# Performance work log

Hardware: AMD Instinct MI355X
Metric: run time of the kernel (lower is better)

## Reference

```python
import jax, jax.numpy as jnp
import numpy as np

_ELECTRODE_POSITIONS = jnp.array([[0.3, 0.25, 0.0], [-0.3, 0.25, 0.0], [-0.05, -0.4, 0.0],
                                  [0.03, 0.05, 0.2], [0.0, 0.05, 0.22], [-0.04, 0.01, 0.21],
                                  [-0.08, -0.02, 0.18], [-0.14, -0.02, 0.13], [-0.2, -0.02, 0.07]],
                                 dtype=jnp.float32)

B, N, T, K, H = 8, 1024, 512, 9, 32


def setup_inputs() -> dict:
    key = jax.random.key(0)
    ks = jax.random.split(key, 9)
    d = jax.random.normal(ks[1], (B, N, 3), jnp.float32)
    d = d / jnp.linalg.norm(d, axis=-1, keepdims=True)  # unit dipole directions
    return {
        'position': jax.random.normal(ks[0], (B, N, 3), jnp.float32) * 0.1,
        'dipole_dir': d,
        'amplitude': jax.random.uniform(ks[2], (B, N), jnp.float32),
        'envelope_t': jax.random.normal(ks[3], (B, N, T), jnp.float32),
        'electrode_offset': jax.random.normal(ks[4], (B, K, 3), jnp.float32) * 0.01,
        'W1': jax.random.normal(ks[5], (H, 7), jnp.float32) * 0.3,
        'b1': jax.random.normal(ks[6], (H,), jnp.float32) * 0.1,
        'W2': jax.random.normal(ks[7], (1, H), jnp.float32) * 0.3,
        'b2': jax.random.normal(ks[8], (1,), jnp.float32) * 0.1,
    }


def _attenuation(position, E, W1, b1, W2, b2):
    # position [B,N,3], E [B,K,3] -> correction [B,N,K]
    pos_exp = jnp.broadcast_to(position[:, :, None, :], (B, N, K, 3))
    r_vec = E[:, None, :, :] - position[:, :, None, :]          # [B,N,K,3]
    r_dist = jnp.maximum(jnp.linalg.norm(r_vec, axis=-1, keepdims=True), 1e-6)
    r_hat = r_vec / r_dist
    feat = jnp.concatenate([pos_exp, r_hat, r_dist], axis=-1)   # [B,N,K,7]
    h = jax.nn.gelu(jnp.einsum('bnkf,hf->bnkh', feat, W1) + b1, approximate=False)
    raw = (jnp.einsum('bnkh,oh->bnko', h, W2) + b2)[..., 0]     # [B,N,K]
    return 1.0 + jnp.tanh(raw) * 0.5


def reference(position, dipole_dir, amplitude, envelope_t, electrode_offset, W1, b1, W2, b2):
    E = _ELECTRODE_POSITIONS[None] + electrode_offset            # [B,K,3]
    amp_env = (amplitude[..., None] * envelope_t)[:, :, None, :]  # [B,N,1,T]
    moment = dipole_dir[..., None] * amp_env                     # [B,N,3,T]
    r_vec = E[:, None, :, :] - position[:, :, None, :]           # [B,N,K,3]
    EPS_SQ = 0.04
    r_dist_sq = jnp.sum(r_vec ** 2, axis=-1)                     # [B,N,K]
    atten_denom = (r_dist_sq + EPS_SQ) ** 1.5
    correction = _attenuation(position, E, W1, b1, W2, b2)       # [B,N,K]
    dot = jnp.einsum('bndt,bnkd->bnkt', moment, r_vec)           # [B,N,K,T]
    V_per_gaussian = dot * (correction / atten_denom)[..., None]
    V_electrodes = jnp.clip(jnp.sum(V_per_gaussian, axis=1), -50.0, 50.0)  # [B,K,T]
    V_RA, V_LA, V_LL = V_electrodes[:, 0], V_electrodes[:, 1], V_electrodes[:, 2]
    V_chest = V_electrodes[:, 3:9]
    WCT = (V_RA + V_LA + V_LL) / 3.0
    leads = jnp.stack([V_LA - V_RA, V_LL - V_RA, V_LL - V_LA,
                       -(V_LA + V_LL) / 2.0 + V_RA,
                       V_LA - (V_RA + V_LL) / 2.0,
                       V_LL - (V_RA + V_LA) / 2.0], axis=1)
    chest_leads = V_chest - WCT[:, None, :]
    v_leads = jnp.concatenate([leads, chest_leads], axis=1)      # [B,12,T]
    return v_leads, V_electrodes
```

## Files before the change

### kernel.cpp

```cpp
#include <hip/hip_runtime.h>
#include <hip/hip_bf16.h>
#include <math.h>

#define BB 8
#define NN 1024
#define TT 512
#define KK 9
#define HH 32

#define NCHUNK 64
#define NPER   (NN/NCHUNK)

__constant__ float c_epos[KK][3] = {
    { 0.30f,  0.25f, 0.00f},
    {-0.30f,  0.25f, 0.00f},
    {-0.05f, -0.40f, 0.00f},
    { 0.03f,  0.05f, 0.20f},
    { 0.00f,  0.05f, 0.22f},
    {-0.04f,  0.01f, 0.21f},
    {-0.08f, -0.02f, 0.18f},
    {-0.14f, -0.02f, 0.13f},
    {-0.20f, -0.02f, 0.07f},
};

__global__ __launch_bounds__(256) void fused_kernel(
    const float* __restrict__ pos,
    const float* __restrict__ dd,
    const float* __restrict__ amp,
    const float* __restrict__ env,
    const float* __restrict__ eoff,
    const float* __restrict__ W1,
    const float* __restrict__ pb1,
    const float* __restrict__ W2,
    const float* __restrict__ pb2,
    float* __restrict__ partial)
{
    const int tid   = threadIdx.x;
    const int chunk = blockIdx.x;
    const int b     = blockIdx.y;
    const int n0    = chunk * NPER;

    __shared__ float sW1[HH * 7];
    __shared__ float sb1[HH];
    __shared__ float sW2[HH];
    __shared__ float sb2;
    __shared__ float sE[KK][3];
    __shared__ float sA[NPER][12];

    if (tid < HH * 7) sW1[tid] = W1[tid];
    if (tid < HH)     { sb1[tid] = pb1[tid]; sW2[tid] = W2[tid]; }
    if (tid < KK * 3) sE[tid / 3][tid % 3] = c_epos[tid / 3][tid % 3] + eoff[b * KK * 3 + tid];
    if (tid == 0)     sb2 = pb2[0];
    __syncthreads();

    if (tid < NPER * KK) {
        const int k  = tid % KK;
        const int nl = tid / KK;
        const int bn = b * NN + n0 + nl;

        const float px = pos[bn * 3 + 0];
        const float py = pos[bn * 3 + 1];
        const float pz = pos[bn * 3 + 2];

        const float rx = sE[k][0] - px, ry = sE[k][1] - py, rz = sE[k][2] - pz;
        const float r2 = rx * rx + ry * ry + rz * rz;
        const float d0 = r2 + 0.04f;
        const float denom = d0 * sqrtf(d0);

        const float rdist = fmaxf(sqrtf(r2), 1e-6f);
        const float rinv  = 1.0f / rdist;
        float feat[7];
        feat[0] = px; feat[1] = py; feat[2] = pz;
        feat[3] = rx * rinv; feat[4] = ry * rinv; feat[5] = rz * rinv;
        feat[6] = rdist;

        float raw = sb2;
        #pragma unroll
        for (int j = 0; j < HH; ++j) {
            float s = sb1[j];
            #pragma unroll
            for (int f = 0; f < 7; ++f) s += sW1[j * 7 + f] * feat[f];
            const float g = 0.5f * s * (1.0f + erff(s * 0.70710678118654752f));
            raw += sW2[j] * g;
        }
        const float corr = 1.0f + 0.5f * tanhf(raw);

        const float ddx = dd[bn * 3 + 0], ddy = dd[bn * 3 + 1], ddz = dd[bn * 3 + 2];
        const float dot = ddx * rx + ddy * ry + ddz * rz;

        sA[nl][k] = amp[bn] * dot * corr / denom;
    }
    __syncthreads();

    float2 acc[KK];
    #pragma unroll
    for (int k = 0; k < KK; ++k) { acc[k].x = 0.0f; acc[k].y = 0.0f; }

    const float2* envp = (const float2*)(env + ((size_t)(b * NN + n0)) * TT) + tid;
    const float4* s4 = (const float4*)sA;
    #pragma unroll
    for (int nl = 0; nl < NPER; ++nl) {
        const float2 ev = envp[(size_t)nl * (TT / 2)];
        const float4 a0 = s4[nl * 3 + 0];
        const float4 a1 = s4[nl * 3 + 1];
        const float  a8 = sA[nl][8];
        acc[0].x += a0.x * ev.x; acc[0].y += a0.x * ev.y;
        acc[1].x += a0.y * ev.x; acc[1].y += a0.y * ev.y;
        acc[2].x += a0.z * ev.x; acc[2].y += a0.z * ev.y;
        acc[3].x += a0.w * ev.x; acc[3].y += a0.w * ev.y;
        acc[4].x += a1.x * ev.x; acc[4].y += a1.x * ev.y;
        acc[5].x += a1.y * ev.x; acc[5].y += a1.y * ev.y;
        acc[6].x += a1.z * ev.x; acc[6].y += a1.z * ev.y;
        acc[7].x += a1.w * ev.x; acc[7].y += a1.w * ev.y;
        acc[8].x += a8   * ev.x; acc[8].y += a8   * ev.y;
    }

    float2* pp = (float2*)(partial + (((size_t)chunk * BB + b) * KK) * TT) + tid;
    #pragma unroll
    for (int k = 0; k < KK; ++k) pp[(size_t)k * (TT / 2)] = acc[k];
}

__global__ __launch_bounds__(256) void finalize_kernel(
    const float* __restrict__ partial,
    float* __restrict__ out)
{
    const int tid = threadIdx.x;
    const int tl4 = tid & 7;
    const int cg  = tid >> 3;
    const int tc  = blockIdx.x;
    const int b   = blockIdx.y;
    const int t0  = tc * 32;

    float4 s[KK];
    #pragma unroll
    for (int k = 0; k < KK; ++k) s[k] = make_float4(0.f, 0.f, 0.f, 0.f);

    #pragma unroll
    for (int ci = 0; ci < 2; ++ci) {
        const int c = cg + 32 * ci;
        const float* base = partial + (((size_t)c * BB + b) * KK) * TT + t0 + tl4 * 4;
        #pragma unroll
        for (int k = 0; k < KK; ++k) {
            const float4 v = *(const float4*)(base + (size_t)k * TT);
            s[k].x += v.x; s[k].y += v.y; s[k].z += v.z; s[k].w += v.w;
        }
    }

    __shared__ float4 sV[32][KK][8];
    __shared__ float  sRf[KK][32];
    #pragma unroll
    for (int k = 0; k < KK; ++k) sV[cg][k][tl4] = s[k];
    __syncthreads();

    if (tid < KK * 8) {
        const int k  = tid >> 3;
        const int tl = tid & 7;
        float4 v = make_float4(0.f, 0.f, 0.f, 0.f);
        #pragma unroll
        for (int g = 0; g < 32; ++g) {
            const float4 u = sV[g][k][tl];
            v.x += u.x; v.y += u.y; v.z += u.z; v.w += u.w;
        }
        sRf[k][tl * 4 + 0] = fminf(fmaxf(v.x, -50.0f), 50.0f);
        sRf[k][tl * 4 + 1] = fminf(fmaxf(v.y, -50.0f), 50.0f);
        sRf[k][tl * 4 + 2] = fminf(fmaxf(v.z, -50.0f), 50.0f);
        sRf[k][tl * 4 + 3] = fminf(fmaxf(v.w, -50.0f), 50.0f);
    }
    __syncthreads();

    if (tid < 32) {
        const int t = t0 + tid;
        float V[KK];
        #pragma unroll
        for (int k = 0; k < KK; ++k) V[k] = sRf[k][tid];

        float* vleads = out;
        float* velec  = out + (size_t)BB * 12 * TT;

        #pragma unroll
        for (int k = 0; k < KK; ++k)
            velec[((size_t)b * KK + k) * TT + t] = V[k];

        const float RA = V[0], LA = V[1], LL = V[2];
        const float WCT = (RA + LA + LL) * (1.0f / 3.0f);

        float L[12];
        L[0] = LA - RA;
        L[1] = LL - RA;
        L[2] = LL - LA;
        L[3] = RA - 0.5f * (LA + LL);
        L[4] = LA - 0.5f * (RA + LL);
        L[5] = LL - 0.5f * (RA + LA);
        L[6]  = V[3] - WCT;
        L[7]  = V[4] - WCT;
        L[8]  = V[5] - WCT;
        L[9]  = V[6] - WCT;
        L[10] = V[7] - WCT;
        L[11] = V[8] - WCT;

        #pragma unroll
        for (int l = 0; l < 12; ++l)
            vleads[((size_t)b * 12 + l) * TT + t] = L[l];
    }
}

extern "C" void kernel_launch(void* const* d_in, const int* in_sizes, int n_in,
                              void* d_out, int out_size, void* d_ws, size_t ws_size,
                              hipStream_t stream) {
    const float* pos  = (const float*)d_in[0];
    const float* dd   = (const float*)d_in[1];
    const float* amp  = (const float*)d_in[2];
    const float* env  = (const float*)d_in[3];
    const float* eoff = (const float*)d_in[4];
    const float* W1   = (const float*)d_in[5];
    const float* b1   = (const float*)d_in[6];
    const float* W2   = (const float*)d_in[7];
    const float* b2   = (const float*)d_in[8];
    float* out = (float*)d_out;

    float* partial = (float*)d_ws;

    {
        dim3 grid(NCHUNK, BB);
        fused_kernel<<<grid, 256, 0, stream>>>(
            pos, dd, amp, env, eoff, W1, b1, W2, b2, partial);
    }
    {
        dim3 grid(16, BB);
        finalize_kernel<<<grid, 256, 0, stream>>>(partial, out);
    }
}
```

Measured before the change: 20.02 us.

## Use 512-thread blocks with two N-groups, prefetch envelope, halve partial chunks

Halves the number of N chunks and doubles the block to 512 threads. Each half of the block accumulates 16 sources for the same time slice, and the two halves are reduced through shared memory before one partial is written. The first 8 envelope rows are now prefetched before the MLP/attenuation barrier so the loads overlap that compute. The finalize kernel reads half as many partials. The risks are fewer blocks in the grid (256 total), an extra barrier, and more shared memory per block.

```diff
diff --git a/kernel.cpp b/kernel.cpp
--- a/kernel.cpp
+++ b/kernel.cpp
@@ -8,7 +8,7 @@
 #define KK 9
 #define HH 32
 
-#define NCHUNK 64
+#define NCHUNK 32
 #define NPER   (NN/NCHUNK)
 
 __constant__ float c_epos[KK][3] = {
@@ -23,7 +23,7 @@
     {-0.20f, -0.02f, 0.07f},
 };
 
-__global__ __launch_bounds__(256) void fused_kernel(
+__global__ __launch_bounds__(512) void fused_kernel(
     const float* __restrict__ pos,
     const float* __restrict__ dd,
     const float* __restrict__ amp,
@@ -39,6 +39,8 @@
     const int chunk = blockIdx.x;
     const int b     = blockIdx.y;
     const int n0    = chunk * NPER;
+    const int ng    = tid >> 8;
+    const int tp    = tid & 255;
 
     __shared__ float sW1[HH * 7];
     __shared__ float sb1[HH];
@@ -46,11 +48,18 @@
     __shared__ float sb2;
     __shared__ float sE[KK][3];
     __shared__ float sA[NPER][12];
+    __shared__ float2 sP[2][KK][256];
 
     if (tid < HH * 7) sW1[tid] = W1[tid];
     if (tid < HH)     { sb1[tid] = pb1[tid]; sW2[tid] = W2[tid]; }
     if (tid < KK * 3) sE[tid / 3][tid % 3] = c_epos[tid / 3][tid % 3] + eoff[b * KK * 3 + tid];
     if (tid == 0)     sb2 = pb2[0];
+
+    const float2* envp = (const float2*)(env + ((size_t)(b * NN + n0 + ng * 16)) * TT) + tp;
+    float2 pf[8];
+    #pragma unroll
+    for (int i = 0; i < 8; ++i) pf[i] = envp[(size_t)i * (TT / 2)];
+
     __syncthreads();
 
     if (tid < NPER * KK) {
@@ -96,11 +105,11 @@
     #pragma unroll
     for (int k = 0; k < KK; ++k) { acc[k].x = 0.0f; acc[k].y = 0.0f; }
 
-    const float2* envp = (const float2*)(env + ((size_t)(b * NN + n0)) * TT) + tid;
     const float4* s4 = (const float4*)sA;
     #pragma unroll
-    for (int nl = 0; nl < NPER; ++nl) {
-        const float2 ev = envp[(size_t)nl * (TT / 2)];
+    for (int i = 0; i < 16; ++i) {
+        const int nl = ng * 16 + i;
+        const float2 ev = (i < 8) ? pf[i] : envp[(size_t)i * (TT / 2)];
         const float4 a0 = s4[nl * 3 + 0];
         const float4 a1 = s4[nl * 3 + 1];
         const float  a8 = sA[nl][8];
@@ -115,9 +124,20 @@
         acc[8].x += a8   * ev.x; acc[8].y += a8   * ev.y;
     }
 
-    float2* pp = (float2*)(partial + (((size_t)chunk * BB + b) * KK) * TT) + tid;
-    #pragma unroll
-    for (int k = 0; k < KK; ++k) pp[(size_t)k * (TT / 2)] = acc[k];
+    #pragma unroll
+    for (int k = 0; k < KK; ++k) sP[ng][k][tp] = acc[k];
+    __syncthreads();
+
+    if (tid < 256) {
+        float2* pp = (float2*)(partial + (((size_t)chunk * BB + b) * KK) * TT) + tp;
+        #pragma unroll
+        for (int k = 0; k < KK; ++k) {
+            const float2 u = sP[0][k][tp];
+            const float2 v = sP[1][k][tp];
+            float2 w; w.x = u.x + v.x; w.y = u.y + v.y;
+            pp[(size_t)k * (TT / 2)] = w;
+        }
+    }
 }
 
 __global__ __launch_bounds__(256) void finalize_kernel(
@@ -132,18 +152,11 @@
     const int t0  = tc * 32;
 
     float4 s[KK];
-    #pragma unroll
-    for (int k = 0; k < KK; ++k) s[k] = make_float4(0.f, 0.f, 0.f, 0.f);
-
-    #pragma unroll
-    for (int ci = 0; ci < 2; ++ci) {
-        const int c = cg + 32 * ci;
-        const float* base = partial + (((size_t)c * BB + b) * KK) * TT + t0 + tl4 * 4;
-        #pragma unroll
-        for (int k = 0; k < KK; ++k) {
-            const float4 v = *(const float4*)(base + (size_t)k * TT);
-            s[k].x += v.x; s[k].y += v.y; s[k].z += v.z; s[k].w += v.w;
-        }
+    {
+        const float* base = partial + (((size_t)cg * BB + b) * KK) * TT + t0 + tl4 * 4;
+        #pragma unroll
+        for (int k = 0; k < KK; ++k)
+            s[k] = *(const float4*)(base + (size_t)k * TT);
     }
 
     __shared__ float4 sV[32][KK][8];
@@ -222,7 +235,7 @@
 
     {
         dim3 grid(NCHUNK, BB);
-        fused_kernel<<<grid, 256, 0, stream>>>(
+        fused_kernel<<<grid, 512, 0, stream>>>(
             pos, dd, amp, env, eoff, W1, b1, W2, b2, partial);
     }
     {
```

After: 18.62 us. 1.08x faster.
